# Kernel tuning notes

Hardware: AMD Instinct MI355X
Metric: run time of the kernel (lower is better)

The kernel has to match this reference:

```python
import jax, jax.numpy as jnp
import numpy as np

NG = 100000   # number of g-side nodes
NS = 100000   # number of s-side nodes
E = 640000    # edges per direction
D = 128       # feature / embed dim


def setup_inputs() -> dict:
    key = jax.random.key(0)
    ks = jax.random.split(key, 16)
    inp = {
        'Xg_self':  jax.random.normal(ks[0], (NG, D), jnp.float32),
        'Xs_self':  jax.random.normal(ks[1], (NS, D), jnp.float32),
        'Xs_for_g': jax.random.normal(ks[2], (NS, D), jnp.float32),
        'Xg_for_s': jax.random.normal(ks[3], (NG, D), jnp.float32),
        # COO edge lists for the two bipartite sparse adjacencies
        'row_gs': jax.random.randint(ks[4], (E,), 0, NG, jnp.int32),
        'col_gs': jax.random.randint(ks[5], (E,), 0, NS, jnp.int32),
        'val_gs': jax.random.uniform(ks[6], (E,), jnp.float32),
        'row_sg': jax.random.randint(ks[7], (E,), 0, NS, jnp.int32),
        'col_sg': jax.random.randint(ks[8], (E,), 0, NG, jnp.int32),
        'val_sg': jax.random.uniform(ks[9], (E,), jnp.float32),
        # Linear weights (PyTorch layout: [out_features, in_features], no bias)
        'Wg_self':  jax.random.normal(ks[10], (D, D), jnp.float32) * 0.05,
        'Wg_neigh': jax.random.normal(ks[11], (D, D), jnp.float32) * 0.05,
        'Ws_self':  jax.random.normal(ks[12], (D, D), jnp.float32) * 0.05,
        'Ws_neigh': jax.random.normal(ks[13], (D, D), jnp.float32) * 0.05,
    }
    return inp


def reference(Xg_self, Xs_self, Xs_for_g, Xg_for_s,
              row_gs, col_gs, val_gs, row_sg, col_sg, val_sg,
              Wg_self, Wg_neigh, Ws_self, Ws_neigh):
    # SpMM: neigh_g = A_gs @ Xs_for_g  (Ng x Ns sparse times Ns x D dense)
    neigh_g = jax.ops.segment_sum(Xs_for_g[col_gs] * val_gs[:, None], row_gs,
                                  num_segments=NG)
    # SpMM: neigh_s = A_sg @ Xg_for_s
    neigh_s = jax.ops.segment_sum(Xg_for_s[col_sg] * val_sg[:, None], row_sg,
                                  num_segments=NS)
    out_g = jax.nn.relu(Xg_self @ Wg_self.T + neigh_g @ Wg_neigh.T)
    out_s = jax.nn.relu(Xs_self @ Ws_self.T + neigh_s @ Ws_neigh.T)
    return (out_g, out_s)
```

## Files before the change

### kernel.cpp

```cpp
#include <hip/hip_runtime.h>
#include <hip/hip_bf16.h>
#include <stdint.h>

typedef __attribute__((ext_vector_type(4))) float f32x4;
typedef __attribute__((ext_vector_type(2))) float f32x2;
typedef __attribute__((ext_vector_type(8))) short bf16x8;

#define D 128
#define GLOBAL_AS __attribute__((address_space(1)))
#define LDS_AS __attribute__((address_space(3)))

__device__ inline short f2bf(float x) {
    __hip_bfloat16 h = __float2bfloat16(x);
    return __builtin_bit_cast(short, h);
}

__device__ inline bf16x8 pack8(f32x4 lo, f32x4 hi) {
    bf16x8 b;
    b[0] = f2bf(lo[0]); b[1] = f2bf(lo[1]); b[2] = f2bf(lo[2]); b[3] = f2bf(lo[3]);
    b[4] = f2bf(hi[0]); b[5] = f2bf(hi[1]); b[6] = f2bf(hi[2]); b[7] = f2bf(hi[3]);
    return b;
}


__global__ __launch_bounds__(256)
void wprep_kernel(const float* __restrict__ Wg_self, const float* __restrict__ Wg_neigh,
                  const float* __restrict__ Ws_self, const float* __restrict__ Ws_neigh,
                  short* __restrict__ Wcat)
{
    int t = blockIdx.x * 256 + threadIdx.x;
    if (t >= 2 * 128 * 32) return;
    int dir = t >> 12;
    int rem = t & 4095;
    int j = rem >> 5;
    int k = (rem & 31) * 8;
    const float* Wself  = dir ? Ws_self  : Wg_self;
    const float* Wneigh = dir ? Ws_neigh : Wg_neigh;
    const float* src = (k < 128) ? (Wself + j * D + k) : (Wneigh + j * D + (k - 128));
    f32x4 lo = *reinterpret_cast<const f32x4*>(src);
    f32x4 hi = *reinterpret_cast<const f32x4*>(src + 4);
    *reinterpret_cast<bf16x8*>(Wcat + (size_t)dir * 32768 + j * 256 + k) = pack8(lo, hi);
}


__global__ __launch_bounds__(256)
void hist2_kernel(const int* __restrict__ rowA, int EA,
                  const int* __restrict__ rowB, int NGoff,
                  int* __restrict__ cnt, int Etot)
{
    int e = blockIdx.x * 256 + threadIdx.x;
    if (e >= Etot) return;
    int r = (e < EA) ? rowA[e] : (rowB[e - EA] + NGoff);
    atomicAdd(&cnt[r], 1);
}

__global__ __launch_bounds__(256)
void scan1_kernel(const int* __restrict__ cnt, int* __restrict__ part,
                  int* __restrict__ blksums, int N)
{
    __shared__ int wsum[4];
    int t = threadIdx.x;
    int base = blockIdx.x * 1024 + t * 4;
    int v0 = base + 0 < N ? cnt[base + 0] : 0;
    int v1 = base + 1 < N ? cnt[base + 1] : 0;
    int v2 = base + 2 < N ? cnt[base + 2] : 0;
    int v3 = base + 3 < N ? cnt[base + 3] : 0;
    int s = v0 + v1 + v2 + v3;
    int lane = t & 63, w = t >> 6;
    int x = s;
#pragma unroll
    for (int off = 1; off < 64; off <<= 1) {
        int y = __shfl_up(x, off);
        if (lane >= off) x += y;
    }
    if (lane == 63) wsum[w] = x;
    __syncthreads();
    int woff = 0;
    for (int i = 0; i < w; ++i) woff += wsum[i];
    int incl = x + woff;
    int excl = incl - s;
    if (base + 0 < N) part[base + 0] = excl;
    if (base + 1 < N) part[base + 1] = excl + v0;
    if (base + 2 < N) part[base + 2] = excl + v0 + v1;
    if (base + 3 < N) part[base + 3] = excl + v0 + v1 + v2;
    if (t == 255) blksums[blockIdx.x] = incl;
}

__global__ __launch_bounds__(256)
void scan2_kernel(int* __restrict__ blksums, int nb)
{
    __shared__ int wsum[4];
    int t = threadIdx.x;
    int v = t < nb ? blksums[t] : 0;
    int lane = t & 63, w = t >> 6;
    int x = v;
#pragma unroll
    for (int off = 1; off < 64; off <<= 1) {
        int y = __shfl_up(x, off);
        if (lane >= off) x += y;
    }
    if (lane == 63) wsum[w] = x;
    __syncthreads();
    int woff = 0;
    for (int i = 0; i < w; ++i) woff += wsum[i];
    int excl = x + woff - v;
    if (t < nb) blksums[t] = excl;
}

__global__ __launch_bounds__(256)
void scan3_kernel(int* __restrict__ start, int* __restrict__ cursor,
                  const int* __restrict__ blksums, int N)
{
    int i = blockIdx.x * 256 + threadIdx.x;
    if (i < N) {
        int v = start[i] + blksums[i >> 10];
        start[i] = v;
        cursor[i] = v;
    }
}

__global__ __launch_bounds__(256)
void fill2_kernel(const int* __restrict__ rowA, const int* __restrict__ colA,
                  const float* __restrict__ valA, int EA,
                  const int* __restrict__ rowB, const int* __restrict__ colB,
                  const float* __restrict__ valB, int NGoff,
                  int* __restrict__ cursor, int2* __restrict__ pairs, int Etot)
{
    int e = blockIdx.x * 256 + threadIdx.x;
    if (e >= Etot) return;
    int r, c; float v;
    if (e < EA) { r = rowA[e]; c = colA[e]; v = valA[e]; }
    else { int e2 = e - EA; r = rowB[e2] + NGoff; c = colB[e2]; v = valB[e2]; }
    int p = atomicAdd(&cursor[r], 1);
    pairs[p] = make_int2(c, __float_as_int(v));
}

__global__ __launch_bounds__(256)
void gather_kernel(const float* __restrict__ X0, const float* __restrict__ X1,
                   const int* __restrict__ start, const int* __restrict__ cnt,
                   const int2* __restrict__ pairs,
                   float* __restrict__ neigh0, float* __restrict__ neigh1,
                   int NG, int N)
{
    int wid = (blockIdx.x * 256 + threadIdx.x) >> 6;
    if (wid >= N) return;
    int lane = threadIdx.x & 63;
    const float* X = (wid < NG) ? X0 : X1;
    float* dst = (wid < NG) ? (neigh0 + (size_t)wid * D)
                            : (neigh1 + (size_t)(wid - NG) * D);
    int s = __builtin_amdgcn_readfirstlane(start[wid]);
    int n = __builtin_amdgcn_readfirstlane(cnt[wid]);
    f32x2 acc = {0.f, 0.f};
    int i = 0;
    for (; i + 8 <= n; i += 8) {
        f32x2 x[8]; float v[8];
#pragma unroll
        for (int u = 0; u < 8; ++u) {
            int2 p = pairs[s + i + u];
            v[u] = __int_as_float(p.y);
            x[u] = *reinterpret_cast<const f32x2*>(X + (size_t)p.x * D + lane * 2);
        }
#pragma unroll
        for (int u = 0; u < 8; ++u) {
            acc[0] += x[u][0] * v[u];
            acc[1] += x[u][1] * v[u];
        }
    }
    for (; i < n; ++i) {
        int2 p = pairs[s + i];
        float v = __int_as_float(p.y);
        f32x2 x = *reinterpret_cast<const f32x2*>(X + (size_t)p.x * D + lane * 2);
        acc[0] += x[0] * v;
        acc[1] += x[1] * v;
    }
    *reinterpret_cast<f32x2*>(dst + lane * 2) = acc;
}

__global__ __launch_bounds__(256)
void gemm_relu_main(const float* __restrict__ Xself0, const float* __restrict__ Neigh0,
                    float* __restrict__ out0, int n0,
                    const float* __restrict__ Xself1, const float* __restrict__ Neigh1,
                    float* __restrict__ out1, int n1,
                    const short* __restrict__ Wcat)
{
    __shared__ float A[32 * 256];
    const int ROWS = 32;
    int blocks0 = (n0 + ROWS - 1) / ROWS;

    const float *Xself, *Neigh; float* out; int nRows, r0base; const short* Wb;
    if ((int)blockIdx.x < blocks0) {
        Xself = Xself0; Neigh = Neigh0; out = out0; nRows = n0;
        r0base = blockIdx.x * ROWS; Wb = Wcat;
    } else {
        Xself = Xself1; Neigh = Neigh1; out = out1; nRows = n1;
        r0base = ((int)blockIdx.x - blocks0) * ROWS; Wb = Wcat + 32768;
    }

    const int tid = threadIdx.x, wave = tid >> 6, lane = tid & 63;
    const int l15 = lane & 15, lhi = lane >> 4;

#pragma unroll
    for (int i = 0; i < 8; ++i) {
        int r = wave * 8 + i;
        int R = r0base + r; if (R > nRows - 1) R = nRows - 1;
        const float* half = (lane < 32) ? (Xself + (size_t)R * D) : (Neigh + (size_t)R * D);
        const float* g = half + (((lane & 31) ^ (r & 7)) << 2);
        __builtin_amdgcn_global_load_lds((const GLOBAL_AS uint32_t*)g,
                                         (LDS_AS uint32_t*)(&A[r * 256]), 16, 0, 0);
    }

    bf16x8 bfrag[2][8];
#pragma unroll
    for (int n = 0; n < 2; ++n) {
        int j = wave * 32 + n * 16 + l15;
#pragma unroll
        for (int kb = 0; kb < 8; ++kb)
            bfrag[n][kb] = *reinterpret_cast<const bf16x8*>(
                Wb + (size_t)j * 256 + kb * 32 + lhi * 8);
    }

    asm volatile("s_waitcnt vmcnt(0)" ::: "memory");
    __syncthreads();

#pragma unroll
    for (int it = 0; it < 2; ++it) {
        int r = it * 16 + l15;
        const float* Arow = &A[r * 256];
        int rx = r & 7;
        f32x4 acc0 = {0.f, 0.f, 0.f, 0.f};
        f32x4 acc1 = {0.f, 0.f, 0.f, 0.f};
#pragma unroll
        for (int kb = 0; kb < 8; ++kb) {
            int c0 = kb * 8 + lhi * 2;
            int m0 = ((c0 & 31) ^ rx) | (c0 & 32);
            int m1 = (((c0 + 1) & 31) ^ rx) | (c0 & 32);
            f32x4 lo = *reinterpret_cast<const f32x4*>(Arow + m0 * 4);
            f32x4 hi = *reinterpret_cast<const f32x4*>(Arow + m1 * 4);
            bf16x8 af = pack8(lo, hi);
            acc0 = __builtin_amdgcn_mfma_f32_16x16x32_bf16(af, bfrag[0][kb], acc0, 0, 0, 0);
            acc1 = __builtin_amdgcn_mfma_f32_16x16x32_bf16(af, bfrag[1][kb], acc1, 0, 0, 0);
        }
#pragma unroll
        for (int i2 = 0; i2 < 4; ++i2) {
            int rr = r0base + it * 16 + lhi * 4 + i2;
            if (rr < nRows) {
                float v0 = acc0[i2] > 0.f ? acc0[i2] : 0.f;
                float v1 = acc1[i2] > 0.f ? acc1[i2] : 0.f;
                out[(size_t)rr * D + wave * 32 + l15]      = v0;
                out[(size_t)rr * D + wave * 32 + 16 + l15] = v1;
            }
        }
    }
}


__global__ __launch_bounds__(256)
void scatter_edges(const float* __restrict__ X, const int* __restrict__ row,
                   const int* __restrict__ col, const float* __restrict__ val,
                   float* out, int nE)
{
    int t = blockIdx.x * 256 + threadIdx.x;
    int e = t >> 5;
    if (e >= nE) return;
    int l = t & 31;
    int r = row[e];
    int c = col[e];
    float v = val[e];
    f32x4 x = *reinterpret_cast<const f32x4*>(X + (size_t)c * D + l * 4);
    float* o = out + (size_t)r * D + l * 4;
    unsafeAtomicAdd(o + 0, x[0] * v);
    unsafeAtomicAdd(o + 1, x[1] * v);
    unsafeAtomicAdd(o + 2, x[2] * v);
    unsafeAtomicAdd(o + 3, x[3] * v);
}

__global__ __launch_bounds__(256)
void gemm_relu_fb(const float* __restrict__ Xself, const float* __restrict__ Neigh,
                  const float* __restrict__ Wself, const float* __restrict__ Wneigh,
                  float* __restrict__ out, int nRows)
{
    const int tid  = threadIdx.x;
    const int wave = tid >> 6;
    const int lane = tid & 63;
    const int l15  = lane & 15;
    const int lhi  = lane >> 4;

    bf16x8 bfrag[2][8];
#pragma unroll
    for (int n = 0; n < 2; ++n) {
        int j = wave * 32 + n * 16 + l15;
#pragma unroll
        for (int kb = 0; kb < 8; ++kb) {
            int k = kb * 32 + lhi * 8;
            const float* src = (kb < 4) ? (Wself + j * D + k)
                                        : (Wneigh + j * D + (k - 128));
            f32x4 lo = *reinterpret_cast<const f32x4*>(src);
            f32x4 hi = *reinterpret_cast<const f32x4*>(src + 4);
            bfrag[n][kb] = pack8(lo, hi);
        }
    }

    int r0base = blockIdx.x * 128;
#pragma unroll 1
    for (int it = 0; it < 8; ++it) {
        int r0 = r0base + it * 16;
        if (r0 >= nRows) break;
        const float* xrow = Xself + (size_t)(r0 + l15) * D;
        const float* nrow = Neigh + (size_t)(r0 + l15) * D;
        bf16x8 afrag[8];
#pragma unroll
        for (int kb = 0; kb < 8; ++kb) {
            const float* src = (kb < 4) ? (xrow + kb * 32 + lhi * 8)
                                        : (nrow + (kb - 4) * 32 + lhi * 8);
            f32x4 lo = *reinterpret_cast<const f32x4*>(src);
            f32x4 hi = *reinterpret_cast<const f32x4*>(src + 4);
            afrag[kb] = pack8(lo, hi);
        }
        asm volatile("s_waitcnt vmcnt(0)" ::: "memory");
        __syncthreads();

        f32x4 acc0 = {0.f, 0.f, 0.f, 0.f};
        f32x4 acc1 = {0.f, 0.f, 0.f, 0.f};
#pragma unroll
        for (int kb = 0; kb < 8; ++kb) {
            acc0 = __builtin_amdgcn_mfma_f32_16x16x32_bf16(afrag[kb], bfrag[0][kb], acc0, 0, 0, 0);
            acc1 = __builtin_amdgcn_mfma_f32_16x16x32_bf16(afrag[kb], bfrag[1][kb], acc1, 0, 0, 0);
        }
#pragma unroll
        for (int i = 0; i < 4; ++i) {
            int rr = r0 + lhi * 4 + i;
            if (rr < nRows) {
                float v0 = acc0[i] > 0.f ? acc0[i] : 0.f;
                float v1 = acc1[i] > 0.f ? acc1[i] : 0.f;
                out[(size_t)rr * D + wave * 32 + l15]      = v0;
                out[(size_t)rr * D + wave * 32 + 16 + l15] = v1;
            }
        }
    }
}


extern "C" void kernel_launch(void* const* d_in, const int* in_sizes, int n_in,
                              void* d_out, int out_size, void* d_ws, size_t ws_size,
                              hipStream_t stream)
{
    const float* Xg_self  = (const float*)d_in[0];
    const float* Xs_self  = (const float*)d_in[1];
    const float* Xs_for_g = (const float*)d_in[2];
    const float* Xg_for_s = (const float*)d_in[3];
    const int*   row_gs   = (const int*)d_in[4];
    const int*   col_gs   = (const int*)d_in[5];
    const float* val_gs   = (const float*)d_in[6];
    const int*   row_sg   = (const int*)d_in[7];
    const int*   col_sg   = (const int*)d_in[8];
    const float* val_sg   = (const float*)d_in[9];
    const float* Wg_self  = (const float*)d_in[10];
    const float* Wg_neigh = (const float*)d_in[11];
    const float* Ws_self  = (const float*)d_in[12];
    const float* Ws_neigh = (const float*)d_in[13];

    const int NG = in_sizes[0] / D;
    const int NS = in_sizes[1] / D;
    const int E1 = in_sizes[4];
    const int E2 = in_sizes[7];
    const int N  = NG + NS;
    const int Etot = E1 + E2;

    float* out_g = (float*)d_out;
    float* out_s = out_g + (size_t)NG * D;

    size_t off = 0;
    auto alloc = [&](size_t bytes) -> size_t {
        off = (off + 255) & ~(size_t)255;
        size_t o = off;
        off += bytes;
        return o;
    };
    size_t wcat_o   = alloc(sizeof(short) * 2 * 128 * 256);
    size_t cnt_o    = alloc(sizeof(int) * N);
    size_t start_o  = alloc(sizeof(int) * N);
    size_t cursor_o = alloc(sizeof(int) * N);
    size_t pairs_o  = alloc(sizeof(int2) * (size_t)Etot);
    size_t blk_o    = alloc(sizeof(int) * 1024);
    size_t csr_bytes = off;
    size_t neigh0_o  = alloc(sizeof(float) * (size_t)NG * D);
    size_t neigh1_o  = alloc(sizeof(float) * (size_t)NS * D);
    size_t full_bytes = off;

    char* ws = (char*)d_ws;
    bool have_csr   = ws_size >= csr_bytes;
    bool have_neigh = ws_size >= full_bytes;

    if (!have_csr) {
        hipMemsetAsync(d_out, 0, (size_t)out_size * sizeof(float), stream);
        {
            long long threads = (long long)E1 * 32;
            scatter_edges<<<(int)((threads + 255) / 256), 256, 0, stream>>>(
                Xs_for_g, row_gs, col_gs, val_gs, out_g, E1);
        }
        {
            long long threads = (long long)E2 * 32;
            scatter_edges<<<(int)((threads + 255) / 256), 256, 0, stream>>>(
                Xg_for_s, row_sg, col_sg, val_sg, out_s, E2);
        }
        gemm_relu_fb<<<(NG + 127) / 128, 256, 0, stream>>>(Xg_self, out_g, Wg_self, Wg_neigh, out_g, NG);
        gemm_relu_fb<<<(NS + 127) / 128, 256, 0, stream>>>(Xs_self, out_s, Ws_self, Ws_neigh, out_s, NS);
        return;
    }

    short* wcat  = (short*)(ws + wcat_o);
    int* cnt     = (int*)(ws + cnt_o);
    int* start   = (int*)(ws + start_o);
    int* cursor  = (int*)(ws + cursor_o);
    int2* pairs  = (int2*)(ws + pairs_o);
    int* blk     = (int*)(ws + blk_o);
    float* neigh0 = have_neigh ? (float*)(ws + neigh0_o) : out_g;
    float* neigh1 = have_neigh ? (float*)(ws + neigh1_o) : out_s;

    wprep_kernel<<<32, 256, 0, stream>>>(Wg_self, Wg_neigh, Ws_self, Ws_neigh, wcat);
    hipMemsetAsync(cnt, 0, sizeof(int) * N, stream);
    hist2_kernel<<<(Etot + 255) / 256, 256, 0, stream>>>(row_gs, E1, row_sg, NG, cnt, Etot);
    int nb = (N + 1023) / 1024;
    scan1_kernel<<<nb, 256, 0, stream>>>(cnt, start, blk, N);
    scan2_kernel<<<1, 256, 0, stream>>>(blk, nb);
    scan3_kernel<<<(N + 255) / 256, 256, 0, stream>>>(start, cursor, blk, N);
    fill2_kernel<<<(Etot + 255) / 256, 256, 0, stream>>>(
        row_gs, col_gs, val_gs, E1, row_sg, col_sg, val_sg, NG, cursor, pairs, Etot);
    gather_kernel<<<(N * 64 + 255) / 256, 256, 0, stream>>>(
        Xs_for_g, Xg_for_s, start, cnt, pairs, neigh0, neigh1, NG, N);

    int blocks0 = (NG + 31) / 32, blocks1 = (NS + 31) / 32;
    gemm_relu_main<<<blocks0 + blocks1, 256, 0, stream>>>(
        Xg_self, neigh0, out_g, NG,
        Xs_self, neigh1, out_s, NS, wcat);
}
```

Measured before the change: 356.3 us.

## Fuse SpMM gather into GEMM kernel and gather from bf16-converted features

Replaces the separate gather kernel and the fp32 neighbour buffers with a fused kernel. Each block gathers neighbour sums for its 32 rows straight into LDS as bf16 and then runs the MFMA GEMM with ReLU. The neighbour feature tables are first converted to bf16 by a new prep kernel, which halves the bytes read by the random gathers. The goal is to drop the neighbour-buffer write and re-read. The costs are an extra conversion pass, bf16 rounding of the gathered inputs, and a gather loop per block that handles rows serially, which may limit memory-level parallelism.

```diff
diff --git a/kernel.cpp b/kernel.cpp
--- a/kernel.cpp
+++ b/kernel.cpp
@@ -7,8 +7,6 @@
 typedef __attribute__((ext_vector_type(8))) short bf16x8;
 
 #define D 128
-#define GLOBAL_AS __attribute__((address_space(1)))
-#define LDS_AS __attribute__((address_space(3)))
 
 __device__ inline short f2bf(float x) {
     __hip_bfloat16 h = __float2bfloat16(x);
@@ -20,6 +18,23 @@
     b[0] = f2bf(lo[0]); b[1] = f2bf(lo[1]); b[2] = f2bf(lo[2]); b[3] = f2bf(lo[3]);
     b[4] = f2bf(hi[0]); b[5] = f2bf(hi[1]); b[6] = f2bf(hi[2]); b[7] = f2bf(hi[3]);
     return b;
+}
+
+__device__ inline unsigned int pack2bf(float a, float b) {
+    unsigned int ua = (unsigned int)(unsigned short)f2bf(a);
+    unsigned int ub = (unsigned int)(unsigned short)f2bf(b);
+    return ua | (ub << 16);
+}
+
+
+__global__ __launch_bounds__(256)
+void xprep_kernel(const float* __restrict__ src, unsigned short* __restrict__ dst, int n8)
+{
+    int i = blockIdx.x * 256 + threadIdx.x;
+    if (i >= n8) return;
+    f32x4 lo = *reinterpret_cast<const f32x4*>(src + (size_t)i * 8);
+    f32x4 hi = *reinterpret_cast<const f32x4*>(src + (size_t)i * 8 + 4);
+    *reinterpret_cast<bf16x8*>(dst + (size_t)i * 8) = pack8(lo, hi);
 }
 
 
@@ -136,77 +151,77 @@
 }
 
 __global__ __launch_bounds__(256)
-void gather_kernel(const float* __restrict__ X0, const float* __restrict__ X1,
-                   const int* __restrict__ start, const int* __restrict__ cnt,
-                   const int2* __restrict__ pairs,
-                   float* __restrict__ neigh0, float* __restrict__ neigh1,
-                   int NG, int N)
-{
-    int wid = (blockIdx.x * 256 + threadIdx.x) >> 6;
-    if (wid >= N) return;
-    int lane = threadIdx.x & 63;
-    const float* X = (wid < NG) ? X0 : X1;
-    float* dst = (wid < NG) ? (neigh0 + (size_t)wid * D)
-                            : (neigh1 + (size_t)(wid - NG) * D);
-    int s = __builtin_amdgcn_readfirstlane(start[wid]);
-    int n = __builtin_amdgcn_readfirstlane(cnt[wid]);
-    f32x2 acc = {0.f, 0.f};
-    int i = 0;
-    for (; i + 8 <= n; i += 8) {
-        f32x2 x[8]; float v[8];
-#pragma unroll
-        for (int u = 0; u < 8; ++u) {
-            int2 p = pairs[s + i + u];
-            v[u] = __int_as_float(p.y);
-            x[u] = *reinterpret_cast<const f32x2*>(X + (size_t)p.x * D + lane * 2);
-        }
-#pragma unroll
-        for (int u = 0; u < 8; ++u) {
-            acc[0] += x[u][0] * v[u];
-            acc[1] += x[u][1] * v[u];
-        }
-    }
-    for (; i < n; ++i) {
-        int2 p = pairs[s + i];
-        float v = __int_as_float(p.y);
-        f32x2 x = *reinterpret_cast<const f32x2*>(X + (size_t)p.x * D + lane * 2);
-        acc[0] += x[0] * v;
-        acc[1] += x[1] * v;
-    }
-    *reinterpret_cast<f32x2*>(dst + lane * 2) = acc;
-}
-
-__global__ __launch_bounds__(256)
-void gemm_relu_main(const float* __restrict__ Xself0, const float* __restrict__ Neigh0,
-                    float* __restrict__ out0, int n0,
-                    const float* __restrict__ Xself1, const float* __restrict__ Neigh1,
-                    float* __restrict__ out1, int n1,
-                    const short* __restrict__ Wcat)
-{
-    __shared__ float A[32 * 256];
+void fused_kernel(const unsigned short* __restrict__ X16_0,
+                  const unsigned short* __restrict__ X16_1,
+                  const float* __restrict__ Xself0, float* __restrict__ out0, int n0,
+                  const float* __restrict__ Xself1, float* __restrict__ out1, int n1,
+                  const int* __restrict__ start, const int* __restrict__ cnt,
+                  const int2* __restrict__ pairs, const short* __restrict__ Wcat)
+{
+    __shared__ bf16x8 Ab[32 * 32];
     const int ROWS = 32;
     int blocks0 = (n0 + ROWS - 1) / ROWS;
 
-    const float *Xself, *Neigh; float* out; int nRows, r0base; const short* Wb;
+    const unsigned short* X16; const float* Xself; float* out;
+    int nRows, r0base, csr0; const short* Wb;
     if ((int)blockIdx.x < blocks0) {
-        Xself = Xself0; Neigh = Neigh0; out = out0; nRows = n0;
-        r0base = blockIdx.x * ROWS; Wb = Wcat;
+        X16 = X16_0; Xself = Xself0; out = out0; nRows = n0;
+        r0base = blockIdx.x * ROWS; csr0 = 0; Wb = Wcat;
     } else {
-        Xself = Xself1; Neigh = Neigh1; out = out1; nRows = n1;
-        r0base = ((int)blockIdx.x - blocks0) * ROWS; Wb = Wcat + 32768;
+        X16 = X16_1; Xself = Xself1; out = out1; nRows = n1;
+        r0base = ((int)blockIdx.x - blocks0) * ROWS; csr0 = n0; Wb = Wcat + 32768;
     }
 
     const int tid = threadIdx.x, wave = tid >> 6, lane = tid & 63;
     const int l15 = lane & 15, lhi = lane >> 4;
-
-#pragma unroll
-    for (int i = 0; i < 8; ++i) {
-        int r = wave * 8 + i;
-        int R = r0base + r; if (R > nRows - 1) R = nRows - 1;
-        const float* half = (lane < 32) ? (Xself + (size_t)R * D) : (Neigh + (size_t)R * D);
-        const float* g = half + (((lane & 31) ^ (r & 7)) << 2);
-        __builtin_amdgcn_global_load_lds((const GLOBAL_AS uint32_t*)g,
-                                         (LDS_AS uint32_t*)(&A[r * 256]), 16, 0, 0);
+    const int l31 = lane & 31, half = lane >> 5;
+
+    unsigned int* Aw   = (unsigned int*)Ab;
+    uint2*        A64  = (uint2*)Ab;
+
+#pragma unroll 1
+    for (int i = 0; i < 4; ++i) {
+        int r = wave * 8 + i * 2 + half;
+        int R = r0base + r;
+        if (R >= nRows) R = nRows - 1;
+        int gid = csr0 + R;
+        int s = start[gid];
+        int n = cnt[gid];
+        f32x4 acc = {0.f, 0.f, 0.f, 0.f};
+        int j = 0;
+        for (; j + 4 <= n; j += 4) {
+            int2 p[4]; uint2 xb[4];
+#pragma unroll
+            for (int u = 0; u < 4; ++u) {
+                p[u] = pairs[s + j + u];
+                xb[u] = *reinterpret_cast<const uint2*>(X16 + (size_t)p[u].x * D + l31 * 4);
+            }
+#pragma unroll
+            for (int u = 0; u < 4; ++u) {
+                float v = __int_as_float(p[u].y);
+                acc[0] += __uint_as_float(xb[u].x << 16) * v;
+                acc[1] += __uint_as_float(xb[u].x & 0xffff0000u) * v;
+                acc[2] += __uint_as_float(xb[u].y << 16) * v;
+                acc[3] += __uint_as_float(xb[u].y & 0xffff0000u) * v;
+            }
+        }
+        for (; j < n; ++j) {
+            int2 p = pairs[s + j];
+            uint2 xb = *reinterpret_cast<const uint2*>(X16 + (size_t)p.x * D + l31 * 4);
+            float v = __int_as_float(p.y);
+            acc[0] += __uint_as_float(xb.x << 16) * v;
+            acc[1] += __uint_as_float(xb.x & 0xffff0000u) * v;
+            acc[2] += __uint_as_float(xb.y << 16) * v;
+            acc[3] += __uint_as_float(xb.y & 0xffff0000u) * v;
+        }
+        f32x4 xs = *reinterpret_cast<const f32x4*>(Xself + (size_t)R * D + l31 * 4);
+        uint2 sb = { pack2bf(xs[0], xs[1]),  pack2bf(xs[2], xs[3]) };
+        uint2 nb = { pack2bf(acc[0], acc[1]), pack2bf(acc[2], acc[3]) };
+        int rx = r & 7;
+        int cS = (l31 >> 1) ^ rx;
+        int cN = 16 + ((l31 >> 1) ^ rx);
+        A64[r * 64 + cS * 2 + (l31 & 1)] = sb;
+        A64[r * 64 + cN * 2 + (l31 & 1)] = nb;
     }
 
     bf16x8 bfrag[2][8];
@@ -219,24 +234,18 @@
                 Wb + (size_t)j * 256 + kb * 32 + lhi * 8);
     }
 
-    asm volatile("s_waitcnt vmcnt(0)" ::: "memory");
     __syncthreads();
 
 #pragma unroll
     for (int it = 0; it < 2; ++it) {
         int r = it * 16 + l15;
-        const float* Arow = &A[r * 256];
         int rx = r & 7;
         f32x4 acc0 = {0.f, 0.f, 0.f, 0.f};
         f32x4 acc1 = {0.f, 0.f, 0.f, 0.f};
 #pragma unroll
         for (int kb = 0; kb < 8; ++kb) {
-            int c0 = kb * 8 + lhi * 2;
-            int m0 = ((c0 & 31) ^ rx) | (c0 & 32);
-            int m1 = (((c0 + 1) & 31) ^ rx) | (c0 & 32);
-            f32x4 lo = *reinterpret_cast<const f32x4*>(Arow + m0 * 4);
-            f32x4 hi = *reinterpret_cast<const f32x4*>(Arow + m1 * 4);
-            bf16x8 af = pack8(lo, hi);
+            int c = kb * 4 + lhi;
+            bf16x8 af = Ab[r * 32 + (c ^ rx)];
             acc0 = __builtin_amdgcn_mfma_f32_16x16x32_bf16(af, bfrag[0][kb], acc0, 0, 0, 0);
             acc1 = __builtin_amdgcn_mfma_f32_16x16x32_bf16(af, bfrag[1][kb], acc1, 0, 0, 0);
         }
@@ -376,22 +385,19 @@
         off += bytes;
         return o;
     };
+    size_t x16g_o   = alloc(sizeof(short) * (size_t)NG * D);
+    size_t x16s_o   = alloc(sizeof(short) * (size_t)NS * D);
     size_t wcat_o   = alloc(sizeof(short) * 2 * 128 * 256);
     size_t cnt_o    = alloc(sizeof(int) * N);
     size_t start_o  = alloc(sizeof(int) * N);
     size_t cursor_o = alloc(sizeof(int) * N);
     size_t pairs_o  = alloc(sizeof(int2) * (size_t)Etot);
     size_t blk_o    = alloc(sizeof(int) * 1024);
-    size_t csr_bytes = off;
-    size_t neigh0_o  = alloc(sizeof(float) * (size_t)NG * D);
-    size_t neigh1_o  = alloc(sizeof(float) * (size_t)NS * D);
-    size_t full_bytes = off;
+    size_t need_bytes = off;
 
     char* ws = (char*)d_ws;
-    bool have_csr   = ws_size >= csr_bytes;
-    bool have_neigh = ws_size >= full_bytes;
-
-    if (!have_csr) {
+
+    if (ws_size < need_bytes) {
         hipMemsetAsync(d_out, 0, (size_t)out_size * sizeof(float), stream);
         {
             long long threads = (long long)E1 * 32;
@@ -408,16 +414,19 @@
         return;
     }
 
+    unsigned short* x16g = (unsigned short*)(ws + x16g_o);
+    unsigned short* x16s = (unsigned short*)(ws + x16s_o);
     short* wcat  = (short*)(ws + wcat_o);
     int* cnt     = (int*)(ws + cnt_o);
     int* start   = (int*)(ws + start_o);
     int* cursor  = (int*)(ws + cursor_o);
     int2* pairs  = (int2*)(ws + pairs_o);
     int* blk     = (int*)(ws + blk_o);
-    float* neigh0 = have_neigh ? (float*)(ws + neigh0_o) : out_g;
-    float* neigh1 = have_neigh ? (float*)(ws + neigh1_o) : out_s;
-
+
+    xprep_kernel<<<(NG * D / 8 + 255) / 256, 256, 0, stream>>>(Xs_for_g, x16g, NG * D / 8);
+    xprep_kernel<<<(NS * D / 8 + 255) / 256, 256, 0, stream>>>(Xg_for_s, x16s, NS * D / 8);
     wprep_kernel<<<32, 256, 0, stream>>>(Wg_self, Wg_neigh, Ws_self, Ws_neigh, wcat);
+
     hipMemsetAsync(cnt, 0, sizeof(int) * N, stream);
     hist2_kernel<<<(Etot + 255) / 256, 256, 0, stream>>>(row_gs, E1, row_sg, NG, cnt, Etot);
     int nb = (N + 1023) / 1024;
@@ -426,11 +435,11 @@
     scan3_kernel<<<(N + 255) / 256, 256, 0, stream>>>(start, cursor, blk, N);
     fill2_kernel<<<(Etot + 255) / 256, 256, 0, stream>>>(
         row_gs, col_gs, val_gs, E1, row_sg, col_sg, val_sg, NG, cursor, pairs, Etot);
-    gather_kernel<<<(N * 64 + 255) / 256, 256, 0, stream>>>(
-        Xs_for_g, Xg_for_s, start, cnt, pairs, neigh0, neigh1, NG, N);
 
     int blocks0 = (NG + 31) / 32, blocks1 = (NS + 31) / 32;
-    gemm_relu_main<<<blocks0 + blocks1, 256, 0, stream>>>(
-        Xg_self, neigh0, out_g, NG,
-        Xs_self, neigh1, out_s, NS, wcat);
-}
+    fused_kernel<<<blocks0 + blocks1, 256, 0, stream>>>(
+        x16g, x16s,
+        Xg_self, out_g, NG,
+        Xs_self, out_s, NS,
+        start, cnt, pairs, wcat);
+}
```

Measured after the change: 319.0 us. 1.12x faster.
